# Performance work log

Hardware: AMD Instinct MI355X
Metric: run time of the kernel (lower is better)

Reference implementation:

```python
import jax, jax.numpy as jnp
import numpy as np

N_NODES = 50000
N_EDGES = 400000
N_GRAPHS = 500
N_FEAT = 4
EMB = 200
HID = 128


def setup_inputs() -> dict:
    key = jax.random.key(0)
    ks = jax.random.split(key, 16)
    x = jax.random.normal(ks[0], (N_NODES, N_FEAT), dtype=jnp.float32)
    edge_index = jax.random.randint(ks[1], (2, N_EDGES), 0, N_NODES, dtype=jnp.int64)
    x_scalar = jax.random.normal(ks[2], (N_GRAPHS, N_FEAT), dtype=jnp.float32)
    batch_index = jnp.sort(jax.random.randint(ks[3], (N_NODES,), 0, N_GRAPHS, dtype=jnp.int64))

    def lin(k, fan_in, fan_out):
        return jax.random.normal(k, (fan_in, fan_out), dtype=jnp.float32) / np.sqrt(fan_in)

    params = {
        'W0': lin(ks[4], N_FEAT, EMB), 'b0': jnp.zeros((EMB,), jnp.float32),
        'W1': lin(ks[5], EMB, EMB), 'b1': jnp.zeros((EMB,), jnp.float32),
        'W2': lin(ks[6], EMB, EMB), 'b2': jnp.zeros((EMB,), jnp.float32),
        'W3': lin(ks[7], EMB, EMB), 'b3': jnp.zeros((EMB,), jnp.float32),
        'Wl1': lin(ks[8], EMB + N_FEAT, HID),
        'bl1': jax.random.normal(ks[9], (HID,), jnp.float32) * 0.01,
        'Wl2': lin(ks[10], HID, 1),
        'bl2': jax.random.normal(ks[11], (1,), jnp.float32) * 0.01,
    }
    return dict(x=x, edge_index=edge_index, x_scalar=x_scalar, batch_index=batch_index, **params)


def _gcn_conv(h, W, b, src, dst, norm, num_nodes):
    # PyG GCNConv: h' = D^-1/2 (A+I) D^-1/2 (h W) + b, with precomputed edge norms
    m = (h @ W)[src] * norm[:, None]            # [E+N, out]
    out = jax.ops.segment_sum(m, dst, num_segments=num_nodes)
    return out + b


def reference(x, edge_index, x_scalar, batch_index,
              W0, b0, W1, b1, W2, b2, W3, b3, Wl1, bl1, Wl2, bl2):
    num_nodes = x.shape[0]
    loops = jnp.arange(num_nodes, dtype=edge_index.dtype)
    src = jnp.concatenate([edge_index[0], loops])  # self-loops appended
    dst = jnp.concatenate([edge_index[1], loops])
    deg = jax.ops.segment_sum(jnp.ones_like(dst, dtype=x.dtype), dst, num_segments=num_nodes)
    dinv = deg ** -0.5                              # deg >= 1 due to self-loops
    norm = dinv[src] * dinv[dst]

    h = jax.nn.leaky_relu(_gcn_conv(x, W0, b0, src, dst, norm, num_nodes), 0.01)
    h = jax.nn.leaky_relu(_gcn_conv(h, W1, b1, src, dst, norm, num_nodes), 0.01)
    h = jax.nn.leaky_relu(_gcn_conv(h, W2, b2, src, dst, norm, num_nodes), 0.01)
    h = jax.nn.leaky_relu(_gcn_conv(h, W3, b3, src, dst, norm, num_nodes), 0.01)

    # global mean pool per graph
    sums = jax.ops.segment_sum(h, batch_index, num_segments=N_GRAPHS)
    cnt = jax.ops.segment_sum(jnp.ones((num_nodes,), h.dtype), batch_index, num_segments=N_GRAPHS)
    pooled = sums / jnp.maximum(cnt, 1.0)[:, None]

    g = jnp.concatenate([pooled, x_scalar], axis=1)   # [G, EMB+4]
    g = jax.nn.leaky_relu(g @ Wl1 + bl1, 0.01)
    out = g @ Wl2 + bl2                                # [G, 1]
    return out
```

## Files before the change

kernel.cpp:

```cpp
#include <hip/hip_runtime.h>
#include <math.h>

#define LEAKY(v) ((v) > 0.0f ? (v) : 0.01f * (v))

typedef _Float16 v8h __attribute__((ext_vector_type(8)));
typedef float v4f __attribute__((ext_vector_type(4)));

__global__ void k_count(const int* __restrict__ ei, int* __restrict__ cnt, int E) {
    int e = blockIdx.x * blockDim.x + threadIdx.x;
    if (e < E) atomicAdd(&cnt[ei[E + e]], 1);
}

__global__ __launch_bounds__(256) void k_scan1(const int* __restrict__ cnt,
                                               int* __restrict__ rowptr,
                                               int* __restrict__ bsum, int n) {
    __shared__ int s[256];
    int t = threadIdx.x, i = blockIdx.x * 256 + t;
    int v = (i < n) ? cnt[i] : 0;
    s[t] = v;
    __syncthreads();
    for (int off = 1; off < 256; off <<= 1) {
        int u = (t >= off) ? s[t - off] : 0;
        __syncthreads();
        s[t] += u;
        __syncthreads();
    }
    if (i < n) rowptr[i] = s[t] - v;
    if (t == 255) bsum[blockIdx.x] = s[255];
}

__global__ __launch_bounds__(256) void k_scan2(int* __restrict__ bsum, int nb) {
    __shared__ int s[256];
    int t = threadIdx.x;
    int v = (t < nb) ? bsum[t] : 0;
    s[t] = v;
    __syncthreads();
    for (int off = 1; off < 256; off <<= 1) {
        int u = (t >= off) ? s[t - off] : 0;
        __syncthreads();
        s[t] += u;
        __syncthreads();
    }
    if (t < nb) bsum[t] = s[t] - v;
}

__global__ __launch_bounds__(256) void k_scan3(int* __restrict__ rowptr,
                                               const int* __restrict__ bsum,
                                               const int* __restrict__ cnt,
                                               float* __restrict__ dinv, int n) {
    int i = blockIdx.x * 256 + threadIdx.x;
    if (i < n) {
        rowptr[i] += bsum[blockIdx.x];
        dinv[i] = rsqrtf(1.0f + (float)cnt[i]);
    }
}

__global__ void k_fill(const int* __restrict__ ei, const float* __restrict__ dinv,
                       int* __restrict__ rowptr, int2* __restrict__ adj, int E) {
    int e = blockIdx.x * blockDim.x + threadIdx.x;
    if (e < E) {
        int s = ei[e], d = ei[E + e];
        int pos = atomicAdd(&rowptr[d], 1);
        adj[pos] = make_int2(s, __float_as_int(dinv[s] * dinv[d]));
    }
}

__global__ __launch_bounds__(256) void k_splitW3(const float* __restrict__ W1,
                                                 const float* __restrict__ W2,
                                                 const float* __restrict__ W3,
                                                 _Float16* __restrict__ th0, _Float16* __restrict__ tl0,
                                                 _Float16* __restrict__ th1, _Float16* __restrict__ tl1,
                                                 _Float16* __restrict__ th2, _Float16* __restrict__ tl2,
                                                 int* __restrict__ cnt, int n) {
    int layer = blockIdx.y;
    const float* W = (layer == 0) ? W1 : (layer == 1) ? W2 : W3;
    _Float16* Wth = (layer == 0) ? th0 : (layer == 1) ? th1 : th2;
    _Float16* Wtl = (layer == 0) ? tl0 : (layer == 1) ? tl1 : tl2;
    int idx = blockIdx.x * blockDim.x + threadIdx.x;
    int gidx = (blockIdx.y * gridDim.x + blockIdx.x) * 256 + threadIdx.x;
    for (int j = gidx; j < n; j += gridDim.x * gridDim.y * 256) cnt[j] = 0;
    if (idx >= 224 * 208) return;
    int k = idx / 208, c = idx - k * 208;
    float v = (k < 200 && c < 200) ? W[k * 200 + c] : 0.0f;
    _Float16 hi = (_Float16)v;
    _Float16 lo = (_Float16)(v - (float)hi);
    Wth[c * 224 + k] = hi;
    Wtl[c * 224 + k] = lo;
}

__global__ __launch_bounds__(256, 4) void k_gemm200_mfma_l0(const float* __restrict__ x,
                                                            const float* __restrict__ dinv,
                                                            const int* __restrict__ rowptr,
                                                            const int2* __restrict__ adj,
                                                            const float* __restrict__ W0,
                                                            const float* __restrict__ b0,
                                                            const _Float16* __restrict__ Wth,
                                                            const _Float16* __restrict__ Wtl,
                                                            _Float16* __restrict__ T, int M) {
    __shared__ _Float16 Wsh[208 * 32];
    __shared__ _Float16 Wsl[208 * 32];
    __shared__ float W0s[4][200];
    __shared__ float b0s[200];
    const int tid  = threadIdx.x;
    const int lane = tid & 63;
    const int wid  = tid >> 6;
    const int quad = lane >> 4;
    const int l16  = lane & 15;
    const int rowA = blockIdx.x * 64 + wid * 16 + l16;
    const int rowAc = min(rowA, M - 1);

    float w0n = dinv[rowAc]; w0n *= w0n;
    float4 xv = ((const float4*)x)[rowAc];
    float4 pxv = make_float4(xv.x * w0n, xv.y * w0n, xv.z * w0n, xv.w * w0n);
    {
        int lo = rowAc ? rowptr[rowAc - 1] : 0;
        int hi = rowptr[rowAc];
        for (int j = lo; j < hi; ++j) {
            int2 cw = adj[j];
            float w = __int_as_float(cw.y);
            float4 sv = ((const float4*)x)[cw.x];
            pxv.x += sv.x * w; pxv.y += sv.y * w; pxv.z += sv.z * w; pxv.w += sv.w * w;
        }
    }

    for (int idx = tid; idx < 1000; idx += 256) {
        if (idx < 800) W0s[idx / 200][idx % 200] = W0[idx];
        else b0s[idx - 800] = b0[idx - 800];
    }
    __syncthreads();

    v4f acc[13];
#pragma unroll
    for (int t = 0; t < 13; ++t) acc[t] = 0.0f;

    for (int k0 = 0; k0 < 224; k0 += 32) {
        v8h ah, al;
        int kb = k0 + quad * 8;
        if (kb < 200) {
#pragma unroll
            for (int j = 0; j < 8; ++j) {
                int k = kb + j;
                float pv = pxv.x * W0s[0][k] + pxv.y * W0s[1][k]
                         + pxv.z * W0s[2][k] + pxv.w * W0s[3][k] + b0s[k];
                pv = LEAKY(pv);
                _Float16 h = (_Float16)pv;
                ah[j] = h;
                al[j] = (_Float16)(pv - (float)h);
            }
        } else {
#pragma unroll
            for (int j = 0; j < 8; ++j) { ah[j] = (_Float16)0.0f; al[j] = (_Float16)0.0f; }
        }
        __syncthreads();
        for (int idx = tid; idx < 832; idx += 256) {
            int nr = idx >> 2, part = idx & 3;
            *(uint4*)&Wsh[nr * 32 + part * 8] = *(const uint4*)&Wth[nr * 224 + k0 + part * 8];
            *(uint4*)&Wsl[nr * 32 + part * 8] = *(const uint4*)&Wtl[nr * 224 + k0 + part * 8];
        }
        __syncthreads();
#pragma unroll
        for (int t = 0; t < 13; ++t) {
            int nidx = (t * 16 + l16) * 32 + quad * 8;
            v8h wh = *(const v8h*)&Wsh[nidx];
            v8h wl = *(const v8h*)&Wsl[nidx];
            acc[t] = __builtin_amdgcn_mfma_f32_16x16x32_f16(ah, wh, acc[t], 0, 0, 0);
            acc[t] = __builtin_amdgcn_mfma_f32_16x16x32_f16(ah, wl, acc[t], 0, 0, 0);
            acc[t] = __builtin_amdgcn_mfma_f32_16x16x32_f16(al, wh, acc[t], 0, 0, 0);
        }
    }
    const int rb = blockIdx.x * 64 + wid * 16 + quad * 4;
#pragma unroll
    for (int t = 0; t < 13; ++t) {
        int c = t * 16 + l16;
        if (c < 200) {
#pragma unroll
            for (int e = 0; e < 4; ++e) {
                int r = rb + e;
                if (r < M) T[(size_t)r * 200 + c] = (_Float16)acc[t][e];
            }
        }
    }
}

__global__ __launch_bounds__(256, 4) void k_gemm200_mfma(const _Float16* __restrict__ P,
                                                         const float* __restrict__ bias,
                                                         const _Float16* __restrict__ Wth,
                                                         const _Float16* __restrict__ Wtl,
                                                         _Float16* __restrict__ T, int M) {
    __shared__ _Float16 Wsh[208 * 32];
    __shared__ _Float16 Wsl[208 * 32];
    const int tid  = threadIdx.x;
    const int lane = tid & 63;
    const int wid  = tid >> 6;
    const int quad = lane >> 4;
    const int l16  = lane & 15;
    const int rowA = blockIdx.x * 64 + wid * 16 + l16;
    const int rowAc = min(rowA, M - 1);
    const _Float16* Prow = P + (size_t)rowAc * 200;

    v4f acc[13];
#pragma unroll
    for (int t = 0; t < 13; ++t) acc[t] = 0.0f;

    for (int k0 = 0; k0 < 224; k0 += 32) {
        v8h ah, al;
        int kb = k0 + quad * 8;
        if (kb < 200) {
            v8h ph = *(const v8h*)(Prow + kb);
            float4 ba = *(const float4*)(bias + kb);
            float4 bb = *(const float4*)(bias + kb + 4);
            float bv[8] = {ba.x, ba.y, ba.z, ba.w, bb.x, bb.y, bb.z, bb.w};
#pragma unroll
            for (int j = 0; j < 8; ++j) {
                float av = (float)ph[j] + bv[j];
                av = LEAKY(av);
                _Float16 h = (_Float16)av;
                ah[j] = h;
                al[j] = (_Float16)(av - (float)h);
            }
        } else {
#pragma unroll
            for (int j = 0; j < 8; ++j) { ah[j] = (_Float16)0.0f; al[j] = (_Float16)0.0f; }
        }
        __syncthreads();
        for (int idx = tid; idx < 832; idx += 256) {
            int nr = idx >> 2, part = idx & 3;
            *(uint4*)&Wsh[nr * 32 + part * 8] = *(const uint4*)&Wth[nr * 224 + k0 + part * 8];
            *(uint4*)&Wsl[nr * 32 + part * 8] = *(const uint4*)&Wtl[nr * 224 + k0 + part * 8];
        }
        __syncthreads();
#pragma unroll
        for (int t = 0; t < 13; ++t) {
            int nidx = (t * 16 + l16) * 32 + quad * 8;
            v8h wh = *(const v8h*)&Wsh[nidx];
            v8h wl = *(const v8h*)&Wsl[nidx];
            acc[t] = __builtin_amdgcn_mfma_f32_16x16x32_f16(ah, wh, acc[t], 0, 0, 0);
            acc[t] = __builtin_amdgcn_mfma_f32_16x16x32_f16(ah, wl, acc[t], 0, 0, 0);
            acc[t] = __builtin_amdgcn_mfma_f32_16x16x32_f16(al, wh, acc[t], 0, 0, 0);
        }
    }
    const int rb = blockIdx.x * 64 + wid * 16 + quad * 4;
#pragma unroll
    for (int t = 0; t < 13; ++t) {
        int c = t * 16 + l16;
        if (c < 200) {
#pragma unroll
            for (int e = 0; e < 4; ++e) {
                int r = rb + e;
                if (r < M) T[(size_t)r * 200 + c] = (_Float16)acc[t][e];
            }
        }
    }
}

__global__ __launch_bounds__(256) void k_gather200h(const _Float16* __restrict__ t,
                                                    const float* __restrict__ dinv,
                                                    const int* __restrict__ rowptr,
                                                    const int2* __restrict__ adj,
                                                    _Float16* __restrict__ p, int n) {
    int gid = blockIdx.x * blockDim.x + threadIdx.x;
    if (gid >= n * 25) return;
    int v = gid / 25, c8 = gid - v * 25;
    const v8h* tp = (const v8h*)t;
    float w0 = dinv[v]; w0 *= w0;
    v8h tv = tp[v * 25 + c8];
    float a0[8], a1[8];
#pragma unroll
    for (int i = 0; i < 8; ++i) { a0[i] = (float)tv[i] * w0; a1[i] = 0.0f; }
    int lo = v ? rowptr[v - 1] : 0;
    int hi = rowptr[v];
    int j = lo;
    for (; j + 1 < hi; j += 2) {
        int2 e0 = adj[j], e1 = adj[j + 1];
        float wa = __int_as_float(e0.y), wb = __int_as_float(e1.y);
        v8h s0 = tp[e0.x * 25 + c8];
        v8h s1 = tp[e1.x * 25 + c8];
#pragma unroll
        for (int i = 0; i < 8; ++i) {
            a0[i] += (float)s0[i] * wa;
            a1[i] += (float)s1[i] * wb;
        }
    }
    if (j < hi) {
        int2 cw = adj[j];
        float w = __int_as_float(cw.y);
        v8h sv = tp[cw.x * 25 + c8];
#pragma unroll
        for (int i = 0; i < 8; ++i) a0[i] += (float)sv[i] * w;
    }
    v8h o;
#pragma unroll
    for (int i = 0; i < 8; ++i) o[i] = (_Float16)(a0[i] + a1[i]);
    ((v8h*)p)[v * 25 + c8] = o;
}

__global__ __launch_bounds__(256) void k_poolg(const _Float16* __restrict__ T,
                                               const float* __restrict__ b3,
                                               const int* __restrict__ batch, int n,
                                               float* __restrict__ pooled) {
    __shared__ float part[10][25][9];
    __shared__ int sb[2];
    int g = blockIdx.x;
    int t = threadIdx.x;
    if (t == 0 || t == 64) {
        int target = g + (t ? 1 : 0);
        int lo = 0, hi = n;
        while (lo < hi) { int m = (lo + hi) >> 1; if (batch[m] < target) lo = m + 1; else hi = m; }
        sb[t ? 1 : 0] = lo;
    }
    __syncthreads();
    int lo = sb[0], hi = sb[1];
    int c8 = t % 25, li = t / 25;
    float acc[8];
#pragma unroll
    for (int i = 0; i < 8; ++i) acc[i] = 0.0f;
    if (li < 10) {
        const v8h* tp = (const v8h*)T;
        float4 ba = *(const float4*)(b3 + c8 * 8);
        float4 bb = *(const float4*)(b3 + c8 * 8 + 4);
        float bv[8] = {ba.x, ba.y, ba.z, ba.w, bb.x, bb.y, bb.z, bb.w};
        for (int i = lo + li; i < hi; i += 10) {
            v8h tv = tp[(size_t)i * 25 + c8];
#pragma unroll
            for (int jj = 0; jj < 8; ++jj) {
                float v = (float)tv[jj] + bv[jj];
                acc[jj] += LEAKY(v);
            }
        }
#pragma unroll
        for (int jj = 0; jj < 8; ++jj) part[li][c8][jj] = acc[jj];
    }
    __syncthreads();
    if (t < 200) {
        int cc8 = t >> 3, jj = t & 7;
        float s = 0.0f;
#pragma unroll
        for (int l2 = 0; l2 < 10; ++l2) s += part[l2][cc8][jj];
        float inv = 1.0f / fmaxf((float)(hi - lo), 1.0f);
        pooled[g * 200 + cc8 * 8 + jj] = s * inv;
    }
}

#define GPB 8
__global__ __launch_bounds__(128) void k_mlpfin(const float* __restrict__ pooled,
                                                const float* __restrict__ xs,
                                                const float* __restrict__ Wl1,
                                                const float* __restrict__ bl1,
                                                const float* __restrict__ Wl2,
                                                const float* __restrict__ bl2,
                                                float* __restrict__ out, int G) {
    __shared__ float Ws[204 * 128];
    __shared__ float growS[204];
    __shared__ float partial[2];
    int t = threadIdx.x;
    for (int idx = t; idx < 204 * 128; idx += 128) Ws[idx] = Wl1[idx];
    float blv = bl1[t], wl2v = Wl2[t], bl2v = bl2[0];
    int g0 = blockIdx.x * GPB;
    for (int gi = 0; gi < GPB; ++gi) {
        int g = g0 + gi;
        if (g >= G) break;
        __syncthreads();
        for (int idx = t; idx < 200; idx += 128) growS[idx] = pooled[g * 200 + idx];
        if (t < 4) growS[200 + t] = xs[g * 4 + t];
        __syncthreads();
        float s = blv;
        for (int k = 0; k < 204; ++k) s += growS[k] * Ws[k * 128 + t];
        s = LEAKY(s);
        float hv = s * wl2v;
        for (int off = 32; off > 0; off >>= 1) hv += __shfl_down(hv, off, 64);
        if ((t & 63) == 0) partial[t >> 6] = hv;
        __syncthreads();
        if (t == 0) out[g] = partial[0] + partial[1] + bl2v;
    }
}

extern "C" void kernel_launch(void* const* d_in, const int* in_sizes, int n_in,
                              void* d_out, int out_size, void* d_ws, size_t ws_size,
                              hipStream_t stream) {
    const float* x    = (const float*)d_in[0];
    const int*   ei   = (const int*)d_in[1];
    const float* xs   = (const float*)d_in[2];
    const int*   batch= (const int*)d_in[3];
    const float* W0   = (const float*)d_in[4];
    const float* b0   = (const float*)d_in[5];
    const float* W1   = (const float*)d_in[6];
    const float* b1   = (const float*)d_in[7];
    const float* W2   = (const float*)d_in[8];
    const float* b2   = (const float*)d_in[9];
    const float* W3   = (const float*)d_in[10];
    const float* b3   = (const float*)d_in[11];
    const float* Wl1  = (const float*)d_in[12];
    const float* bl1  = (const float*)d_in[13];
    const float* Wl2  = (const float*)d_in[14];
    const float* bl2  = (const float*)d_in[15];
    float* out = (float*)d_out;

    const int N = in_sizes[0] / 4;
    const int E = in_sizes[1] / 2;
    const int G = in_sizes[2] / 4;

    char* ws = (char*)d_ws;
    size_t off = 0;
    auto alloc = [&](size_t bytes) { void* p = ws + off; off += (bytes + 255) & ~size_t(255); return p; };
    _Float16* bufA = (_Float16*)alloc((size_t)N * 200 * sizeof(_Float16));
    _Float16* bufB = (_Float16*)alloc((size_t)N * 200 * sizeof(_Float16));
    float* dinv   = (float*)alloc((size_t)N * sizeof(float));
    float* pooled = (float*)alloc((size_t)G * 200 * sizeof(float));
    int*   cnt    = (int*)alloc((size_t)N * sizeof(int));
    int*   rowptr = (int*)alloc(((size_t)N + 1) * sizeof(int));
    int*   bsum   = (int*)alloc(256 * sizeof(int));
    int2*  adj    = (int2*)alloc((size_t)E * sizeof(int2));
    _Float16* Wth[3]; _Float16* Wtl[3];
    for (int i = 0; i < 3; ++i) {
        Wth[i] = (_Float16*)alloc(208 * 224 * sizeof(_Float16));
        Wtl[i] = (_Float16*)alloc(208 * 224 * sizeof(_Float16));
    }

    const int B = 256;
    const int nblk = (N + 255) / 256;

    dim3 sg((224 * 208 + B - 1) / B, 3);
    k_splitW3<<<sg, B, 0, stream>>>(W1, W2, W3, Wth[0], Wtl[0], Wth[1], Wtl[1], Wth[2], Wtl[2],
                                    cnt, N);

    k_count<<<(E + B - 1) / B, B, 0, stream>>>(ei, cnt, E);
    k_scan1<<<nblk, 256, 0, stream>>>(cnt, rowptr, bsum, N);
    k_scan2<<<1, 256, 0, stream>>>(bsum, nblk);
    k_scan3<<<nblk, 256, 0, stream>>>(rowptr, bsum, cnt, dinv, N);
    k_fill<<<(E + B - 1) / B, B, 0, stream>>>(ei, dinv, rowptr, adj, E);

    const int gblocks = (N * 25 + 255) / 256;

    k_gemm200_mfma_l0<<<(N + 63) / 64, 256, 0, stream>>>(x, dinv, rowptr, adj, W0, b0,
                                                         Wth[0], Wtl[0], bufA, N);
    k_gather200h<<<gblocks, 256, 0, stream>>>(bufA, dinv, rowptr, adj, bufB, N);

    k_gemm200_mfma<<<(N + 63) / 64, 256, 0, stream>>>(bufB, b1, Wth[1], Wtl[1], bufA, N);
    k_gather200h<<<gblocks, 256, 0, stream>>>(bufA, dinv, rowptr, adj, bufB, N);
    k_gemm200_mfma<<<(N + 63) / 64, 256, 0, stream>>>(bufB, b2, Wth[2], Wtl[2], bufA, N);
    k_gather200h<<<gblocks, 256, 0, stream>>>(bufA, dinv, rowptr, adj, bufB, N);

    k_poolg<<<G, 256, 0, stream>>>(bufB, b3, batch, N, pooled);
    k_mlpfin<<<(G + GPB - 1) / GPB, 128, 0, stream>>>(pooled, xs, Wl1, bl1, Wl2, bl2, out, G);
}
```

Before: 367.2 us.

## Enlarge GEMM blocks, unroll gather by four, fuse pooling with MLP head

The MFMA GEMM kernels now run 512-thread blocks over 128 rows, so each staged weight tile in shared memory serves twice as many rows. The neighbour gather loop is unrolled to four independent accumulators to keep more loads in flight. Mean pooling and the two-layer MLP head are merged into one kernel, which drops a launch and the pooled intermediate buffer. The trade-offs are fewer resident blocks per CU for the GEMMs and a head that reads Wl1 from global memory per graph instead of through shared memory.

```diff
diff --git a/kernel.cpp b/kernel.cpp
--- a/kernel.cpp
+++ b/kernel.cpp
@@ -88,7 +88,7 @@
     Wtl[c * 224 + k] = lo;
 }
 
-__global__ __launch_bounds__(256, 4) void k_gemm200_mfma_l0(const float* __restrict__ x,
+__global__ __launch_bounds__(512, 2) void k_gemm200_mfma_l0(const float* __restrict__ x,
                                                             const float* __restrict__ dinv,
                                                             const int* __restrict__ rowptr,
                                                             const int2* __restrict__ adj,
@@ -106,7 +106,7 @@
     const int wid  = tid >> 6;
     const int quad = lane >> 4;
     const int l16  = lane & 15;
-    const int rowA = blockIdx.x * 64 + wid * 16 + l16;
+    const int rowA = blockIdx.x * 128 + wid * 16 + l16;
     const int rowAc = min(rowA, M - 1);
 
     float w0n = dinv[rowAc]; w0n *= w0n;
@@ -123,7 +123,7 @@
         }
     }
 
-    for (int idx = tid; idx < 1000; idx += 256) {
+    for (int idx = tid; idx < 1000; idx += 512) {
         if (idx < 800) W0s[idx / 200][idx % 200] = W0[idx];
         else b0s[idx - 800] = b0[idx - 800];
     }
@@ -152,7 +152,7 @@
             for (int j = 0; j < 8; ++j) { ah[j] = (_Float16)0.0f; al[j] = (_Float16)0.0f; }
         }
         __syncthreads();
-        for (int idx = tid; idx < 832; idx += 256) {
+        for (int idx = tid; idx < 832; idx += 512) {
             int nr = idx >> 2, part = idx & 3;
             *(uint4*)&Wsh[nr * 32 + part * 8] = *(const uint4*)&Wth[nr * 224 + k0 + part * 8];
             *(uint4*)&Wsl[nr * 32 + part * 8] = *(const uint4*)&Wtl[nr * 224 + k0 + part * 8];
@@ -168,7 +168,7 @@
             acc[t] = __builtin_amdgcn_mfma_f32_16x16x32_f16(al, wh, acc[t], 0, 0, 0);
         }
     }
-    const int rb = blockIdx.x * 64 + wid * 16 + quad * 4;
+    const int rb = blockIdx.x * 128 + wid * 16 + quad * 4;
 #pragma unroll
     for (int t = 0; t < 13; ++t) {
         int c = t * 16 + l16;
@@ -182,7 +182,7 @@
     }
 }
 
-__global__ __launch_bounds__(256, 4) void k_gemm200_mfma(const _Float16* __restrict__ P,
+__global__ __launch_bounds__(512, 2) void k_gemm200_mfma(const _Float16* __restrict__ P,
                                                          const float* __restrict__ bias,
                                                          const _Float16* __restrict__ Wth,
                                                          const _Float16* __restrict__ Wtl,
@@ -194,7 +194,7 @@
     const int wid  = tid >> 6;
     const int quad = lane >> 4;
     const int l16  = lane & 15;
-    const int rowA = blockIdx.x * 64 + wid * 16 + l16;
+    const int rowA = blockIdx.x * 128 + wid * 16 + l16;
     const int rowAc = min(rowA, M - 1);
     const _Float16* Prow = P + (size_t)rowAc * 200;
 
@@ -223,7 +223,7 @@
             for (int j = 0; j < 8; ++j) { ah[j] = (_Float16)0.0f; al[j] = (_Float16)0.0f; }
         }
         __syncthreads();
-        for (int idx = tid; idx < 832; idx += 256) {
+        for (int idx = tid; idx < 832; idx += 512) {
             int nr = idx >> 2, part = idx & 3;
             *(uint4*)&Wsh[nr * 32 + part * 8] = *(const uint4*)&Wth[nr * 224 + k0 + part * 8];
             *(uint4*)&Wsl[nr * 32 + part * 8] = *(const uint4*)&Wtl[nr * 224 + k0 + part * 8];
@@ -239,7 +239,7 @@
             acc[t] = __builtin_amdgcn_mfma_f32_16x16x32_f16(al, wh, acc[t], 0, 0, 0);
         }
     }
-    const int rb = blockIdx.x * 64 + wid * 16 + quad * 4;
+    const int rb = blockIdx.x * 128 + wid * 16 + quad * 4;
 #pragma unroll
     for (int t = 0; t < 13; ++t) {
         int c = t * 16 + l16;
@@ -264,24 +264,29 @@
     const v8h* tp = (const v8h*)t;
     float w0 = dinv[v]; w0 *= w0;
     v8h tv = tp[v * 25 + c8];
-    float a0[8], a1[8];
-#pragma unroll
-    for (int i = 0; i < 8; ++i) { a0[i] = (float)tv[i] * w0; a1[i] = 0.0f; }
+    float a0[8], a1[8], a2[8], a3[8];
+#pragma unroll
+    for (int i = 0; i < 8; ++i) { a0[i] = (float)tv[i] * w0; a1[i] = 0.0f; a2[i] = 0.0f; a3[i] = 0.0f; }
     int lo = v ? rowptr[v - 1] : 0;
     int hi = rowptr[v];
     int j = lo;
-    for (; j + 1 < hi; j += 2) {
-        int2 e0 = adj[j], e1 = adj[j + 1];
+    for (; j + 3 < hi; j += 4) {
+        int2 e0 = adj[j], e1 = adj[j + 1], e2 = adj[j + 2], e3 = adj[j + 3];
         float wa = __int_as_float(e0.y), wb = __int_as_float(e1.y);
+        float wc = __int_as_float(e2.y), wd = __int_as_float(e3.y);
         v8h s0 = tp[e0.x * 25 + c8];
         v8h s1 = tp[e1.x * 25 + c8];
+        v8h s2 = tp[e2.x * 25 + c8];
+        v8h s3 = tp[e3.x * 25 + c8];
 #pragma unroll
         for (int i = 0; i < 8; ++i) {
             a0[i] += (float)s0[i] * wa;
             a1[i] += (float)s1[i] * wb;
-        }
-    }
-    if (j < hi) {
+            a2[i] += (float)s2[i] * wc;
+            a3[i] += (float)s3[i] * wd;
+        }
+    }
+    for (; j < hi; ++j) {
         int2 cw = adj[j];
         float w = __int_as_float(cw.y);
         v8h sv = tp[cw.x * 25 + c8];
@@ -290,15 +295,22 @@
     }
     v8h o;
 #pragma unroll
-    for (int i = 0; i < 8; ++i) o[i] = (_Float16)(a0[i] + a1[i]);
+    for (int i = 0; i < 8; ++i) o[i] = (_Float16)((a0[i] + a1[i]) + (a2[i] + a3[i]));
     ((v8h*)p)[v * 25 + c8] = o;
 }
 
-__global__ __launch_bounds__(256) void k_poolg(const _Float16* __restrict__ T,
-                                               const float* __restrict__ b3,
-                                               const int* __restrict__ batch, int n,
-                                               float* __restrict__ pooled) {
+__global__ __launch_bounds__(256) void k_poolhead(const _Float16* __restrict__ T,
+                                                  const float* __restrict__ b3,
+                                                  const int* __restrict__ batch, int n,
+                                                  const float* __restrict__ xs,
+                                                  const float* __restrict__ Wl1,
+                                                  const float* __restrict__ bl1,
+                                                  const float* __restrict__ Wl2,
+                                                  const float* __restrict__ bl2,
+                                                  float* __restrict__ out) {
     __shared__ float part[10][25][9];
+    __shared__ float grow[204];
+    __shared__ float partial[2];
     __shared__ int sb[2];
     int g = blockIdx.x;
     int t = threadIdx.x;
@@ -311,14 +323,14 @@
     __syncthreads();
     int lo = sb[0], hi = sb[1];
     int c8 = t % 25, li = t / 25;
-    float acc[8];
-#pragma unroll
-    for (int i = 0; i < 8; ++i) acc[i] = 0.0f;
     if (li < 10) {
         const v8h* tp = (const v8h*)T;
         float4 ba = *(const float4*)(b3 + c8 * 8);
         float4 bb = *(const float4*)(b3 + c8 * 8 + 4);
         float bv[8] = {ba.x, ba.y, ba.z, ba.w, bb.x, bb.y, bb.z, bb.w};
+        float acc[8];
+#pragma unroll
+        for (int i = 0; i < 8; ++i) acc[i] = 0.0f;
         for (int i = lo + li; i < hi; i += 10) {
             v8h tv = tp[(size_t)i * 25 + c8];
 #pragma unroll
@@ -332,46 +344,24 @@
     }
     __syncthreads();
     if (t < 200) {
-        int cc8 = t >> 3, jj = t & 7;
         float s = 0.0f;
 #pragma unroll
-        for (int l2 = 0; l2 < 10; ++l2) s += part[l2][cc8][jj];
-        float inv = 1.0f / fmaxf((float)(hi - lo), 1.0f);
-        pooled[g * 200 + cc8 * 8 + jj] = s * inv;
-    }
-}
-
-#define GPB 8
-__global__ __launch_bounds__(128) void k_mlpfin(const float* __restrict__ pooled,
-                                                const float* __restrict__ xs,
-                                                const float* __restrict__ Wl1,
-                                                const float* __restrict__ bl1,
-                                                const float* __restrict__ Wl2,
-                                                const float* __restrict__ bl2,
-                                                float* __restrict__ out, int G) {
-    __shared__ float Ws[204 * 128];
-    __shared__ float growS[204];
-    __shared__ float partial[2];
-    int t = threadIdx.x;
-    for (int idx = t; idx < 204 * 128; idx += 128) Ws[idx] = Wl1[idx];
-    float blv = bl1[t], wl2v = Wl2[t], bl2v = bl2[0];
-    int g0 = blockIdx.x * GPB;
-    for (int gi = 0; gi < GPB; ++gi) {
-        int g = g0 + gi;
-        if (g >= G) break;
-        __syncthreads();
-        for (int idx = t; idx < 200; idx += 128) growS[idx] = pooled[g * 200 + idx];
-        if (t < 4) growS[200 + t] = xs[g * 4 + t];
-        __syncthreads();
-        float s = blv;
-        for (int k = 0; k < 204; ++k) s += growS[k] * Ws[k * 128 + t];
+        for (int l2 = 0; l2 < 10; ++l2) s += part[l2][t >> 3][t & 7];
+        grow[t] = s / fmaxf((float)(hi - lo), 1.0f);
+    } else if (t < 204) {
+        grow[t] = xs[g * 4 + (t - 200)];
+    }
+    __syncthreads();
+    if (t < 128) {
+        float s = bl1[t];
+        for (int k = 0; k < 204; ++k) s += grow[k] * Wl1[k * 128 + t];
         s = LEAKY(s);
-        float hv = s * wl2v;
+        float hv = s * Wl2[t];
         for (int off = 32; off > 0; off >>= 1) hv += __shfl_down(hv, off, 64);
         if ((t & 63) == 0) partial[t >> 6] = hv;
-        __syncthreads();
-        if (t == 0) out[g] = partial[0] + partial[1] + bl2v;
-    }
+    }
+    __syncthreads();
+    if (t == 0) out[g] = partial[0] + partial[1] + bl2[0];
 }
 
 extern "C" void kernel_launch(void* const* d_in, const int* in_sizes, int n_in,
@@ -405,7 +395,6 @@
     _Float16* bufA = (_Float16*)alloc((size_t)N * 200 * sizeof(_Float16));
     _Float16* bufB = (_Float16*)alloc((size_t)N * 200 * sizeof(_Float16));
     float* dinv   = (float*)alloc((size_t)N * sizeof(float));
-    float* pooled = (float*)alloc((size_t)G * 200 * sizeof(float));
     int*   cnt    = (int*)alloc((size_t)N * sizeof(int));
     int*   rowptr = (int*)alloc(((size_t)N + 1) * sizeof(int));
     int*   bsum   = (int*)alloc(256 * sizeof(int));
@@ -430,16 +419,16 @@
     k_fill<<<(E + B - 1) / B, B, 0, stream>>>(ei, dinv, rowptr, adj, E);
 
     const int gblocks = (N * 25 + 255) / 256;
-
-    k_gemm200_mfma_l0<<<(N + 63) / 64, 256, 0, stream>>>(x, dinv, rowptr, adj, W0, b0,
-                                                         Wth[0], Wtl[0], bufA, N);
+    const int mblocks = (N + 127) / 128;
+
+    k_gemm200_mfma_l0<<<mblocks, 512, 0, stream>>>(x, dinv, rowptr, adj, W0, b0,
+                                                   Wth[0], Wtl[0], bufA, N);
     k_gather200h<<<gblocks, 256, 0, stream>>>(bufA, dinv, rowptr, adj, bufB, N);
 
-    k_gemm200_mfma<<<(N + 63) / 64, 256, 0, stream>>>(bufB, b1, Wth[1], Wtl[1], bufA, N);
+    k_gemm200_mfma<<<mblocks, 512, 0, stream>>>(bufB, b1, Wth[1], Wtl[1], bufA, N);
     k_gather200h<<<gblocks, 256, 0, stream>>>(bufA, dinv, rowptr, adj, bufB, N);
-    k_gemm200_mfma<<<(N + 63) / 64, 256, 0, stream>>>(bufB, b2, Wth[2], Wtl[2], bufA, N);
+    k_gemm200_mfma<<<mblocks, 512, 0, stream>>>(bufB, b2, Wth[2], Wtl[2], bufA, N);
     k_gather200h<<<gblocks, 256, 0, stream>>>(bufA, dinv, rowptr, adj, bufB, N);
 
-    k_poolg<<<G, 256, 0, stream>>>(bufB, b3, batch, N, pooled);
-    k_mlpfin<<<(G + GPB - 1) / GPB, 128, 0, stream>>>(pooled, xs, Wl1, bl1, Wl2, bl2, out, G);
-}
+    k_poolhead<<<G, 256, 0, stream>>>(bufB, b3, batch, N, xs, Wl1, bl1, Wl2, bl2, out);
+}
```

Measured after the change: 337.3 us. 1.09x faster.
